# Kernel optimization log

Hardware: AMD Instinct MI355X
Metric: run time of the kernel (lower is better)

## Reference

```python
import jax, jax.numpy as jnp
import numpy as np

IN_CH = 128
HID = 64
EPS = 1e-5
N_NODES = 20000
E_UND = 80000


def _build_line_graph(edge_index, num_nodes):
    # dedupe to unique undirected edges (src<dst); line-graph nodes = these edges
    src = np.asarray(edge_index[0]); dst = np.asarray(edge_index[1])
    m = src < dst
    u, v = src[m], dst[m]
    key = u.astype(np.int64) * num_nodes + v.astype(np.int64)
    _, first = np.unique(key, return_index=True)
    u, v = u[first], v[first]
    E = u.shape[0]
    # incidence lists grouped by node; all ordered pairs of co-incident edges
    nodes = np.concatenate([u, v])
    eids = np.concatenate([np.arange(E), np.arange(E)])
    order = np.argsort(nodes, kind="stable")
    nodes_s, eids_s = nodes[order], eids[order]
    counts = np.bincount(nodes_s, minlength=num_nodes)
    offsets = np.concatenate([np.zeros(1, np.int64), np.cumsum(counts)])
    grp_start = offsets[nodes_s]
    reps = counts[nodes_s]
    total = int(reps.sum())
    starts = np.cumsum(reps) - reps
    idx = np.arange(total) - np.repeat(starts, reps) + np.repeat(grp_start, reps)
    row = np.repeat(eids_s, reps); col = eids_s[idx]
    keep = row != col
    return np.stack([u, v]), np.stack([row[keep], col[keep]])


def _gcn_conv(x, src, dst, W, b):
    # PyG GCNConv: add self loops, symmetric D^-1/2 (A+I) D^-1/2 normalization
    N = x.shape[0]
    sl = jnp.arange(N)
    s = jnp.concatenate([src, sl]); d = jnp.concatenate([dst, sl])
    deg = jax.ops.segment_sum(jnp.ones(s.shape[0], x.dtype), d, num_segments=N)
    dinv = jax.lax.rsqrt(jnp.maximum(deg, 1.0))
    h = x @ W
    msg = h[s] * (dinv[s] * dinv[d])[:, None]
    return jax.ops.segment_sum(msg, d, num_segments=N) + b


def _edge_scores(line_x, lsrc, ldst, W1, b1, gamma1, beta1, W2, b2):
    h = _gcn_conv(line_x, lsrc, ldst, W1, b1)
    mu = h.mean(0); var = h.var(0)  # BatchNorm1d, training-mode batch stats
    h = jax.nn.relu(gamma1 * (h - mu) * jax.lax.rsqrt(var + EPS) + beta1)
    return jax.nn.sigmoid(_gcn_conv(h, lsrc, ldst, W2, b2))[:, 0]


def _cluster(clean, topk_idx, num_nodes):
    ti = np.asarray(topk_idx)
    sel_src = np.asarray(clean[0])[ti]; sel_dst = np.asarray(clean[1])[ti]
    n2c = np.arange(num_nodes)
    rev = sel_dst[::-1]
    _, fi = np.unique(rev, return_index=True)
    last = sel_dst.shape[0] - 1 - fi
    n2c[sel_dst[last]] = sel_src[last]
    uniq = np.unique(n2c)
    M = int(uniq.shape[0])
    old_to_new = np.full(num_nodes, -1, np.int64)
    old_to_new[uniq] = np.arange(M)
    return old_to_new[n2c], uniq, M


def _make_graph():
    rng = np.random.default_rng(0)
    a = rng.integers(0, N_NODES, E_UND)
    off = rng.integers(1, N_NODES, E_UND)
    b = (a + off) % N_NODES  # no self loops
    u = np.minimum(a, b); v = np.maximum(a, b)
    return np.stack([np.concatenate([u, v]), np.concatenate([v, u])]).astype(np.int64)


def _make_params():
    ks = jax.random.split(jax.random.key(0), 4)
    x = jax.random.normal(ks[0], (N_NODES, IN_CH), jnp.float32)
    W1 = jax.random.normal(ks[1], (IN_CH, HID), jnp.float32) / np.float32(np.sqrt(IN_CH))
    b1 = jnp.zeros((HID,), jnp.float32)
    gamma1 = jnp.ones((HID,), jnp.float32)
    beta1 = jnp.zeros((HID,), jnp.float32)
    W2 = jax.random.normal(ks[2], (HID, 1), jnp.float32) / np.float32(np.sqrt(HID))
    b2 = jnp.zeros((1,), jnp.float32)
    return x, W1, b1, gamma1, beta1, W2, b2


def setup_inputs() -> dict:
    x, W1, b1, gamma1, beta1, W2, b2 = _make_params()
    return {
        "x": x, "W1": W1, "b1": b1, "gamma1": gamma1, "beta1": beta1,
        "W2": W2, "b2": b2,
        "edge_index": jnp.asarray(_make_graph()),
        "batch": jnp.zeros((N_NODES,), jnp.int32),
    }


def reference(x, W1, b1, gamma1, beta1, W2, b2, edge_index, batch):
    N = x.shape[0]
    clean, line_ei = _build_line_graph(edge_index, N)
    csrc = jnp.asarray(clean[0]); cdst = jnp.asarray(clean[1])
    lsrc = jnp.asarray(line_ei[0]); ldst = jnp.asarray(line_ei[1])
    line_x = 0.5 * (x[csrc] + x[cdst])  # line-graph node features
    scores = _edge_scores(line_x, lsrc, ldst, W1, b1, gamma1, beta1, W2, b2)
    E_c = scores.shape[0]
    k = max(1, min(E_c // 2, N // 2))
    _, topk_idx = jax.lax.top_k(scores, k)
    new_indices, uniq, M = _cluster(clean, topk_idx, N)
    ni = jnp.asarray(new_indices)
    # aggregate: per-cluster mean of member node features (code's weights are unused)
    counts = jax.ops.segment_sum(jnp.ones(N, x.dtype), ni, num_segments=M)
    x_pool = jax.ops.segment_sum(x, ni, num_segments=M) / counts[:, None]
    batch_pool = batch[jnp.asarray(uniq)]
    # build_new_edges: relabel, drop self loops, coalesce (sorted unique)
    ei = np.asarray(edge_index)
    ns = new_indices[ei[0]]; nd = new_indices[ei[1]]
    keep = ns != nd
    pk = ns[keep] * M + nd[keep]
    upk = np.unique(pk)
    edge_index_pool = jnp.asarray(np.stack([upk // M, upk % M]))
    return (x_pool, edge_index_pool, batch_pool, scores, ni)
```

## Files before the change

kernel.cpp:

```cpp
#include <hip/hip_runtime.h>
#include <stdint.h>

typedef unsigned long long u64;
typedef unsigned int u32;

#define NND 20000
#define EUA 160000
#define EFE 80000
#define ICH 128
#define HIDC 64
#define SCAN_BS 256
#define NB_N ((NND + 255) / 256)
#define NB_EU ((EUA + 255) / 256)
#define NB_EF ((EFE + 255) / 256)
#define NB_E64 ((EFE * HIDC + 255) / 256)
#define NB_X ((NND * ICH + 255) / 256)
#define NSCAN_B ((NND + SCAN_BS - 1) / SCAN_BS)
#define HIST_BLOCKS 128
#define GEB 64
#define XS_PAD 132
#define NCHAIN 4096
#define OUT_MAX_INIT 3000000
#define BK64 64
#define SEL_BINS 4096


__global__ void kScanA(const int* __restrict__ in, int* __restrict__ out,
                       int* __restrict__ bsums, int n) {
    __shared__ int sh[SCAN_BS];
    int tid = threadIdx.x;
    int i = blockIdx.x * SCAN_BS + tid;
    int v = (i < n) ? in[i] : 0;
    sh[tid] = v;
    __syncthreads();
    for (int o = 1; o < SCAN_BS; o <<= 1) {
        int t = (tid >= o) ? sh[tid - o] : 0;
        __syncthreads();
        sh[tid] += t;
        __syncthreads();
    }
    if (i < n) out[i] = sh[tid] - v;
    if (tid == SCAN_BS - 1) bsums[blockIdx.x] = sh[tid];
}
__global__ void kScanB(int* __restrict__ out, const int* __restrict__ bsums,
                       int n, int nb, int* __restrict__ totalDst) {
    __shared__ int sh[160];
    int tid = threadIdx.x;
    if (tid <= nb) sh[tid] = (tid < nb) ? bsums[tid] : 0;
    __syncthreads();
    if (tid == 0) {
        int acc = 0;
        for (int i = 0; i < nb; i++) { int t = sh[i]; sh[i] = acc; acc += t; }
        sh[nb] = acc;
    }
    __syncthreads();
    int i = blockIdx.x * SCAN_BS + tid;
    if (i < n) out[i] += sh[blockIdx.x];
    if (i == 0) {
        int tot = sh[nb];
        out[n] = tot;
        *totalDst = tot;
    }
}

__global__ void kFilterScatter64(const int* __restrict__ ei, int* __restrict__ cnt,
                                 int* __restrict__ bucketV) {
    int i = blockIdx.x * 256 + threadIdx.x;
    if (i >= EUA) return;
    int s = ei[i], d = ei[EUA + i];
    if (s < d) {
        int p = atomicAdd(&cnt[s], 1);
        bucketV[(s << 6) + p] = d;
    }
}
__global__ void kRankSort64(const int* __restrict__ in, int* __restrict__ out,
                            const int* __restrict__ lenA, int* __restrict__ ucnt) {
    int a = blockIdx.x;
    int len = lenA[a];
    int base = a << 6;
    for (int j = threadIdx.x; j < len; j += 64) {
        int v = in[base + j];
        int r = 0;
        for (int i = 0; i < len; i++) {
            int w = in[base + i];
            r += (w < v) || (w == v && i < j);
        }
        out[base + r] = v;
    }
    __syncthreads();
    int c = 0;
    for (int j = threadIdx.x; j < len; j += 64)
        c += (j == 0) || (out[base + j] != out[base + j - 1]);
#pragma unroll
    for (int o = 32; o > 0; o >>= 1) c += __shfl_down(c, o, 64);
    if (threadIdx.x == 0) ucnt[a] = c;
}
__global__ void kCompactInc(const int* __restrict__ arr, const int* __restrict__ cnt,
                            const int* __restrict__ uoff, int* __restrict__ eU,
                            int* __restrict__ eV, int* __restrict__ icnt) {
    int u = blockIdx.x * 256 + threadIdx.x;
    if (u >= NND) return;
    int s = u << 6, e = s + cnt[u], o = uoff[u];
    int myc = 0;
    for (int i = s; i < e; i++)
        if (i == s || arr[i] != arr[i - 1]) {
            int v = arr[i];
            eU[o] = u; eV[o] = v; o++;
            atomicAdd(&icnt[v], 1);
            myc++;
        }
    if (myc) atomicAdd(&icnt[u], myc);
}

__global__ void kIncScatterDinv64(const int* __restrict__ eU, const int* __restrict__ eV,
                                  const int* __restrict__ scal, int* __restrict__ itmp,
                                  int* __restrict__ ilist, const int* __restrict__ icnt,
                                  float* __restrict__ dinv) {
    int e = blockIdx.x * 256 + threadIdx.x;
    if (e >= scal[0]) return;
    int u = eU[e], v = eV[e];
    ilist[(u << 6) + atomicAdd(&itmp[u], 1)] = e;
    ilist[(v << 6) + atomicAdd(&itmp[v], 1)] = e;
    dinv[e] = rsqrtf((float)(icnt[u] + icnt[v] - 1));
}

__global__ void kGemm(const float* __restrict__ x, const float* __restrict__ W1,
                      const int* __restrict__ eU, const int* __restrict__ eV,
                      const int* __restrict__ scal, float* __restrict__ h) {
    __shared__ float W1s[ICH][HIDC];
    __shared__ float xs[GEB][XS_PAD];
    int t = threadIdx.x;
    int E = scal[0];
    int e0 = blockIdx.x * GEB;
    if (e0 >= E) return;

    {
        const float4* Wv = (const float4*)W1;
        float4* Ws = (float4*)&W1s[0][0];
        for (int i = t; i < ICH * HIDC / 4; i += 256) Ws[i] = Wv[i];
    }
    {
        int eb = t >> 2, q = t & 3;
        int e = e0 + eb;
        if (e < E) {
            int u = eU[e], v = eV[e];
            const float4* xu = (const float4*)(x + (size_t)u * ICH) + q * 8;
            const float4* xv = (const float4*)(x + (size_t)v * ICH) + q * 8;
            float* xd = &xs[eb][q * 32];
#pragma unroll
            for (int i = 0; i < 8; i++) {
                float4 a = xu[i], b = xv[i];
                xd[i * 4 + 0] = 0.5f * (a.x + b.x);
                xd[i * 4 + 1] = 0.5f * (a.y + b.y);
                xd[i * 4 + 2] = 0.5f * (a.z + b.z);
                xd[i * 4 + 3] = 0.5f * (a.w + b.w);
            }
        }
    }
    __syncthreads();

    int cg4 = (t & 15) * 4;
    int es = t >> 4;
    float a00=0,a01=0,a02=0,a03=0, a10=0,a11=0,a12=0,a13=0;
    float a20=0,a21=0,a22=0,a23=0, a30=0,a31=0,a32=0,a33=0;
#pragma unroll 4
    for (int k = 0; k < ICH; k++) {
        float4 wv = *(const float4*)&W1s[k][cg4];
        float x0 = xs[es][k], x1 = xs[es + 16][k];
        float x2 = xs[es + 32][k], x3 = xs[es + 48][k];
        a00 += x0 * wv.x; a01 += x0 * wv.y; a02 += x0 * wv.z; a03 += x0 * wv.w;
        a10 += x1 * wv.x; a11 += x1 * wv.y; a12 += x1 * wv.z; a13 += x1 * wv.w;
        a20 += x2 * wv.x; a21 += x2 * wv.y; a22 += x2 * wv.z; a23 += x2 * wv.w;
        a30 += x3 * wv.x; a31 += x3 * wv.y; a32 += x3 * wv.z; a33 += x3 * wv.w;
    }
    int e;
    e = e0 + es;
    if (e < E) *(float4*)&h[(size_t)e * HIDC + cg4] = make_float4(a00, a01, a02, a03);
    e = e0 + es + 16;
    if (e < E) *(float4*)&h[(size_t)e * HIDC + cg4] = make_float4(a10, a11, a12, a13);
    e = e0 + es + 32;
    if (e < E) *(float4*)&h[(size_t)e * HIDC + cg4] = make_float4(a20, a21, a22, a23);
    e = e0 + es + 48;
    if (e < E) *(float4*)&h[(size_t)e * HIDC + cg4] = make_float4(a30, a31, a32, a33);
}

__global__ void kSGather(const float* __restrict__ h, const float* __restrict__ dinv,
                         const int* __restrict__ icnt, const int* __restrict__ ilist,
                         float* __restrict__ S) {
    int n = blockIdx.x;
    int c = threadIdx.x;
    int base = n << 6, len = icnt[n];
    float acc = 0.f;
    for (int j = 0; j < len; j++) {
        int ed = ilist[base + j];
        acc += h[(size_t)ed * HIDC + c] * dinv[ed];
    }
    S[(size_t)n * HIDC + c] = acc;
}
__global__ void kConv1Red1(const float* __restrict__ h, const float* __restrict__ S,
                           const float* __restrict__ dinv, const int* __restrict__ eU,
                           const int* __restrict__ eV, const float* __restrict__ b1,
                           const int* __restrict__ scal, float* __restrict__ h2,
                           float* __restrict__ partial) {
    int t = threadIdx.x;
    int g = blockIdx.x * 4 + (t >> 6);
    int c = t & 63;
    int E = scal[0];
    float bc = b1[c];
    float acc = 0.f;
    for (int e = g; e < E; e += NCHAIN) {
        float a = dinv[e];
        float v = a * (S[(size_t)eU[e] * HIDC + c] + S[(size_t)eV[e] * HIDC + c]) -
                  a * a * h[(size_t)e * HIDC + c] + bc;
        h2[(size_t)e * HIDC + c] = v;
        acc += v;
    }
    partial[g * HIDC + c] = acc;
}
__global__ void kRed1v(const float* __restrict__ h2, const int* __restrict__ scal,
                       const float* __restrict__ muvar, float* __restrict__ partial) {
    int t = threadIdx.x;
    int g = blockIdx.x * 4 + (t >> 6);
    int c = t & 63;
    int E = scal[0];
    float m = muvar[c];
    float acc = 0.f;
    for (int e = g; e < E; e += NCHAIN) {
        float d = h2[(size_t)e * HIDC + c] - m;
        acc += d * d;
    }
    partial[g * HIDC + c] = acc;
}
__global__ void kRed2(const float* __restrict__ partial, const int* __restrict__ scal,
                      float* __restrict__ muvar, int pass) {
    __shared__ float sh[4][HIDC];
    int t = threadIdx.x;
    int q = t >> 6, c = t & 63;
    float acc = 0.f;
    int g0 = q * (NCHAIN / 4);
    for (int g = g0; g < g0 + NCHAIN / 4; g++) acc += partial[g * HIDC + c];
    sh[q][c] = acc;
    __syncthreads();
    if (q == 0) {
        float s = ((sh[0][c] + sh[1][c]) + sh[2][c]) + sh[3][c];
        muvar[pass * HIDC + c] = s / (float)scal[0];
    }
}
__global__ void kNormZ(const float* __restrict__ h2, const float* __restrict__ muvar,
                       const float* __restrict__ gamma1, const float* __restrict__ beta1,
                       const float* __restrict__ W2, const int* __restrict__ scal,
                       float* __restrict__ z) {
    int idx = blockIdx.x * 256 + threadIdx.x;
    int e = idx >> 6;
    if (e >= scal[0]) return;
    int c = idx & 63;
    float t = gamma1[c] * (h2[idx] - muvar[c]) * rsqrtf(muvar[HIDC + c] + 1e-5f) + beta1[c];
    t = t > 0.f ? t : 0.f;
    float p = t * W2[c];
#pragma unroll
    for (int o = 32; o > 0; o >>= 1) p += __shfl_down(p, o, 64);
    if (c == 0) z[e] = p;
}
__global__ void kS2(const float* __restrict__ z, const float* __restrict__ dinv,
                    const int* __restrict__ icnt, const int* __restrict__ ilist,
                    float* __restrict__ S2) {
    int n = blockIdx.x * 256 + threadIdx.x;
    if (n >= NND) return;
    int base = n << 6, len = icnt[n];
    float acc = 0.f;
    for (int j = 0; j < len; j++) {
        int e = ilist[base + j];
        acc += z[e] * dinv[e];
    }
    S2[n] = acc;
}
__global__ void kScore(const float* __restrict__ z, const float* __restrict__ S2,
                       const float* __restrict__ dinv, const int* __restrict__ eU,
                       const int* __restrict__ eV, const float* __restrict__ b2,
                       const int* __restrict__ scal, float* __restrict__ score,
                       u64* __restrict__ okey, u64* __restrict__ minOkey) {
    int e = blockIdx.x * 256 + threadIdx.x;
    if (e < NND) minOkey[e] = ~0ULL;
    int E = scal[0];
    if (e >= E) return;
    float a = dinv[e];
    float l = a * (S2[eU[e]] + S2[eV[e]]) - a * a * z[e] + b2[0];
    float s = 1.f / (1.f + expf(-l));
    score[e] = s;
    u32 b = __float_as_uint(s);
    b = (b >> 31) ? ~b : (b | 0x80000000u);
    okey[e] = (((u64)b) << 17) | (u32)(0x1FFFFu - (u32)e);
}

__device__ __forceinline__ u64 selReplay(const int* __restrict__ histBase, int passes,
                                         int E, int t, int* aux, int* shTmp) {
    int kr = E / 2;
    if (kr > NND / 2) kr = NND / 2;
    if (kr < 1) kr = 1;
    u64 pref = 1ULL << 48;
    for (int q = 0; q < passes; q++) {
        int shift = 36 - 12 * q;
        const int* hq = histBase + q * SEL_BINS;
        int b[16];
        int g = 0;
#pragma unroll
        for (int j = 0; j < 16; j++) { b[j] = hq[16 * t + j]; g += b[j]; }
        aux[t] = g;
        __syncthreads();
        for (int o = 1; o < 256; o <<= 1) {
            int v = (t + o < 256) ? aux[t + o] : 0;
            __syncthreads();
            aux[t] += v;
            __syncthreads();
        }
        int suf = aux[t] - g;
        if (suf < kr && kr <= suf + g) {
            int cum = suf, found = 16 * t;
            for (int j = 15; j >= 0; j--) {
                int hc = b[j];
                if (cum + hc >= kr) { found = 16 * t + j; break; }
                cum += hc;
            }
            shTmp[0] = found;
            shTmp[1] = kr - cum;
        }
        __syncthreads();
        pref |= ((u64)shTmp[0]) << shift;
        kr = shTmp[1];
        __syncthreads();
    }
    return pref;
}
__global__ void kHistR(const u64* __restrict__ okey, const int* __restrict__ scal,
                       int* __restrict__ histBase, int pass) {
    __shared__ int sh[4][SEL_BINS];
    __shared__ int aux[256];
    __shared__ int shTmp[2];
    int t = threadIdx.x;
    int E = scal[0];
    u64 p = selReplay(histBase, pass, E, t, aux, shTmp);
    for (int j = t; j < 4 * SEL_BINS; j += 256) ((int*)sh)[j] = 0;
    __syncthreads();
    int wv = t >> 6;
    int shift = 36 - 12 * pass;
    u64 maskHi = (~0ULL) << (shift + 12);
    for (int e = blockIdx.x * 256 + t; e < E; e += HIST_BLOCKS * 256) {
        u64 kk = okey[e];
        if ((kk & maskHi) == p)
            atomicAdd(&sh[wv][(int)((kk >> shift) & (SEL_BINS - 1))], 1);
    }
    __syncthreads();
    int* hp = histBase + pass * SEL_BINS;
    for (int j = t; j < SEL_BINS; j += 256) {
        int v = sh[0][j] + sh[1][j] + sh[2][j] + sh[3][j];
        if (v) atomicAdd(&hp[j], v);
    }
}

__global__ void kMinKey(const u64* __restrict__ okey, const int* __restrict__ eV,
                        const int* __restrict__ scal, const int* __restrict__ histBase,
                        u64* __restrict__ minOkey) {
    __shared__ int aux[256];
    __shared__ int shTmp[2];
    int t = threadIdx.x;
    int E = scal[0];
    u64 pref = selReplay(histBase, 4, E, t, aux, shTmp);
    int i = blockIdx.x * 256 + t;
    if (i < E) {
        u64 k = okey[i];
        if (k >= pref) atomicMin(&minOkey[eV[i]], k);
    }
}
__global__ void kCluster(const u64* __restrict__ minOkey, const int* __restrict__ eU,
                         int* __restrict__ n2c, int* __restrict__ present) {
    int v = blockIdx.x * 256 + threadIdx.x;
    if (v >= NND) return;
    u64 mk = minOkey[v];
    int m = v;
    if (mk != ~0ULL) m = eU[0x1FFFFu - (u32)(mk & 0x1FFFFu)];
    n2c[v] = m;
    present[m] = 1;
}

__global__ void kNiXacc(const float* __restrict__ x, const int* __restrict__ n2c,
                        const int* __restrict__ o2n, int* __restrict__ ni,
                        int* __restrict__ ccnt, float* __restrict__ dout) {
    int idx = blockIdx.x * 256 + threadIdx.x;
    if (idx >= NND * ICH) return;
    int n = idx >> 7, c = idx & 127;
    int m = o2n[n2c[n]];
    atomicAdd(&dout[(size_t)m * ICH + c], x[idx]);
    if (c == 0) {
        ni[n] = m;
        atomicAdd(&ccnt[m], 1);
    }
}
__global__ void kXdivCEcount(float* __restrict__ dout, const int* __restrict__ ccnt,
                             const int* __restrict__ scal, const int* __restrict__ ei,
                             const int* __restrict__ ni, int* __restrict__ ecnt2) {
    int idx = blockIdx.x * 256 + threadIdx.x;
    if (idx < scal[2] * ICH) dout[idx] /= (float)ccnt[idx >> 7];
    if (idx < EUA) {
        int a = ni[ei[idx]], b = ni[ei[EUA + idx]];
        if (a != b) atomicAdd(&ecnt2[a], 1);
    }
}

__global__ void kCEscatter(const int* __restrict__ ei, const int* __restrict__ ni,
                           const int* __restrict__ eoff2, int* __restrict__ etmp2,
                           int* __restrict__ bkD) {
    int i = blockIdx.x * 256 + threadIdx.x;
    if (i >= EUA) return;
    int a = ni[ei[i]], b = ni[ei[EUA + i]];
    if (a != b) {
        int p = eoff2[a] + atomicAdd(&etmp2[a], 1);
        bkD[p] = b;
    }
}
__global__ void kRankSort(const int* __restrict__ in, int* __restrict__ out,
                          const int* __restrict__ offA, int* __restrict__ ucnt) {
    int a = blockIdx.x;
    int s = offA[a], e = offA[a + 1], len = e - s;
    for (int j = threadIdx.x; j < len; j += 64) {
        int v = in[s + j];
        int r = 0;
        for (int i = 0; i < len; i++) {
            int w = in[s + i];
            r += (w < v) || (w == v && i < j);
        }
        out[s + r] = v;
    }
    __syncthreads();
    int c = 0;
    for (int j = threadIdx.x; j < len; j += 64)
        c += (j == 0) || (out[s + j] != out[s + j - 1]);
#pragma unroll
    for (int o = 32; o > 0; o >>= 1) c += __shfl_down(c, o, 64);
    if (threadIdx.x == 0) ucnt[a] = c;
}
__global__ void kCEwriteTail(const int* __restrict__ bkD2, const int* __restrict__ eoff2,
                             const int* __restrict__ ueoff, const int* __restrict__ scal,
                             const int* __restrict__ batch, const int* __restrict__ present,
                             const int* __restrict__ o2n, const float* __restrict__ score,
                             const int* __restrict__ ni, float* __restrict__ dout) {
    int i = blockIdx.x * 256 + threadIdx.x;
    int E = scal[0], M = scal[2], Ep = scal[3];
    size_t base = (size_t)M * ICH;
    if (i < NND) {
        int s = eoff2[i], e = eoff2[i + 1];
        float* r0 = dout + base;
        float* r1 = r0 + Ep;
        int o = ueoff[i];
        for (int j = s; j < e; j++)
            if (j == s || bkD2[j] != bkD2[j - 1]) {
                r0[o] = (float)i;
                r1[o] = (float)bkD2[j];
                o++;
            }
    }
    size_t tb = base + 2 * (size_t)Ep;
    if (i < NND && present[i]) dout[tb + o2n[i]] = (float)batch[i];
    if (i < E) dout[tb + M + i] = score[i];
    if (i < NND) dout[tb + M + E + i] = (float)ni[i];
}

extern "C" void kernel_launch(void* const* d_in, const int* in_sizes, int n_in,
                              void* d_out, int out_size, void* d_ws, size_t ws_size,
                              hipStream_t stream) {
    (void)in_sizes; (void)n_in; (void)ws_size;
    const float* x = (const float*)d_in[0];
    const float* W1 = (const float*)d_in[1];
    const float* b1 = (const float*)d_in[2];
    const float* gamma1 = (const float*)d_in[3];
    const float* beta1 = (const float*)d_in[4];
    const float* W2 = (const float*)d_in[5];
    const float* b2 = (const float*)d_in[6];
    const int* ei = (const int*)d_in[7];
    const int* batch = (const int*)d_in[8];
    float* dout = (float*)d_out;

    char* w = (char*)d_ws;
    size_t off = 0;
    auto carve = [&](size_t bytes) -> void* {
        off = (off + 255) & ~(size_t)255;
        void* p = w + off;
        off += bytes;
        return p;
    };
    char* zero0 = w;
    int* cnt = (int*)carve(NND * 4);
    int* itmp = (int*)carve(NND * 4);
    int* icnt = (int*)carve(NND * 4);
    int* present = (int*)carve(NND * 4);
    int* ccnt = (int*)carve(NND * 4);
    int* ecnt2 = (int*)carve(NND * 4);
    int* etmp2 = (int*)carve(NND * 4);
    int* scal = (int*)carve(16 * 4);
    int* hist4 = (int*)carve((size_t)4 * SEL_BINS * 4);
    size_t zeroBytes = off;
    int* ucnt = (int*)carve(NND * 4);
    int* uoff = (int*)carve((NND + 2) * 4);
    int* bsums = (int*)carve((NSCAN_B + 2) * 4);
    int* n2c = (int*)carve(NND * 4);
    int* o2n = (int*)carve((NND + 2) * 4);
    int* niArr = (int*)carve(NND * 4);
    int* eoff2 = (int*)carve((NND + 2) * 4);
    int* uecnt = (int*)carve(NND * 4);
    int* ueoff = (int*)carve((NND + 2) * 4);
    int* bucketV = (int*)carve((size_t)NND * BK64 * 4);
    int* bucketS = (int*)carve((size_t)NND * BK64 * 4);
    int* eU = (int*)carve(EFE * 4);
    int* eV = (int*)carve(EFE * 4);
    int* ilist = (int*)carve((size_t)NND * BK64 * 4);
    int* ilistS = (int*)carve((size_t)NND * BK64 * 4);
    int* bkD = (int*)carve(EUA * 4);
    int* bkD2 = (int*)carve(EUA * 4);
    u64* okey = (u64*)carve(EFE * 8);
    u64* minOkey = (u64*)carve(NND * 8);
    float* dinv = (float*)carve(EFE * 4);
    float* h = (float*)carve((size_t)EFE * HIDC * 4);
    float* h2 = (float*)carve((size_t)EFE * HIDC * 4);
    float* Snode = (float*)carve((size_t)NND * HIDC * 4);
    float* partial = (float*)carve((size_t)NCHAIN * HIDC * 4);
    float* muvar = (float*)carve(128 * 4);
    float* zArr = (float*)carve(EFE * 4);
    float* S2 = (float*)carve(NND * 4);
    float* score = (float*)carve(EFE * 4);

    auto scan = [&](const int* in, int* outp, int* totalDst) {
        kScanA<<<NSCAN_B, SCAN_BS, 0, stream>>>(in, outp, bsums, NND);
        kScanB<<<NSCAN_B, SCAN_BS, 0, stream>>>(outp, bsums, NND, NSCAN_B, totalDst);
    };

    size_t outInit = (size_t)out_size;
    if (outInit > OUT_MAX_INIT) outInit = OUT_MAX_INIT;
    hipMemsetAsync(zero0, 0, zeroBytes, stream);
    hipMemsetAsync(d_out, 0, outInit * 4, stream);

    kFilterScatter64<<<NB_EU, 256, 0, stream>>>(ei, cnt, bucketV);
    kRankSort64<<<NND, 64, 0, stream>>>(bucketV, bucketS, cnt, ucnt);
    scan(ucnt, uoff, scal + 0);
    kCompactInc<<<NB_N, 256, 0, stream>>>(bucketS, cnt, uoff, eU, eV, icnt);

    kIncScatterDinv64<<<NB_EF, 256, 0, stream>>>(eU, eV, scal, itmp, ilist, icnt, dinv);
    kRankSort64<<<NND, 64, 0, stream>>>(ilist, ilistS, icnt, ucnt);

    kGemm<<<(EFE + GEB - 1) / GEB, 256, 0, stream>>>(x, W1, eU, eV, scal, h);
    kSGather<<<NND, HIDC, 0, stream>>>(h, dinv, icnt, ilistS, Snode);
    kConv1Red1<<<NCHAIN / 4, 256, 0, stream>>>(h, Snode, dinv, eU, eV, b1, scal, h2, partial);
    kRed2<<<1, 256, 0, stream>>>(partial, scal, muvar, 0);
    kRed1v<<<NCHAIN / 4, 256, 0, stream>>>(h2, scal, muvar, partial);
    kRed2<<<1, 256, 0, stream>>>(partial, scal, muvar, 1);
    kNormZ<<<NB_E64, 256, 0, stream>>>(h2, muvar, gamma1, beta1, W2, scal, zArr);

    kS2<<<NB_N, 256, 0, stream>>>(zArr, dinv, icnt, ilistS, S2);
    kScore<<<NB_EF, 256, 0, stream>>>(zArr, S2, dinv, eU, eV, b2, scal, score, okey,
                                      minOkey);

    for (int p = 0; p < 4; p++)
        kHistR<<<HIST_BLOCKS, 256, 0, stream>>>(okey, scal, hist4, p);

    kMinKey<<<NB_EF, 256, 0, stream>>>(okey, eV, scal, hist4, minOkey);
    kCluster<<<NB_N, 256, 0, stream>>>(minOkey, eU, n2c, present);
    scan(present, o2n, scal + 2);
    kNiXacc<<<NB_X, 256, 0, stream>>>(x, n2c, o2n, niArr, ccnt, dout);
    kXdivCEcount<<<NB_X, 256, 0, stream>>>(dout, ccnt, scal, ei, niArr, ecnt2);

    scan(ecnt2, eoff2, scal + 4);
    kCEscatter<<<NB_EU, 256, 0, stream>>>(ei, niArr, eoff2, etmp2, bkD);
    kRankSort<<<NND, 64, 0, stream>>>(bkD, bkD2, eoff2, uecnt);
    scan(uecnt, ueoff, scal + 3);
    kCEwriteTail<<<NB_EF, 256, 0, stream>>>(bkD2, eoff2, ueoff, scal, batch, present,
                                            o2n, score, niArr, dout);
}
```

Baseline: 398.0 us.

## Replace atomic cluster feature pooling with per-cluster member-list gather

kCluster now also appends each node to a fixed-capacity (64-slot) member list of its cluster, reusing the bucketV buffer. A new kXPool kernel, one block per cluster, gathers and averages member rows directly. This replaces the per-element float atomicAdd scatter and the separate divide pass, and it removes the full output memset. The risks are overflow if a cluster ever has more than 64 members, and output padding that is no longer zeroed.

```diff
diff --git a/kernel.cpp b/kernel.cpp
--- a/kernel.cpp
+++ b/kernel.cpp
@@ -14,13 +14,11 @@
 #define NB_EU ((EUA + 255) / 256)
 #define NB_EF ((EFE + 255) / 256)
 #define NB_E64 ((EFE * HIDC + 255) / 256)
-#define NB_X ((NND * ICH + 255) / 256)
 #define NSCAN_B ((NND + SCAN_BS - 1) / SCAN_BS)
 #define HIST_BLOCKS 128
 #define GEB 64
 #define XS_PAD 132
 #define NCHAIN 4096
-#define OUT_MAX_INIT 3000000
 #define BK64 64
 #define SEL_BINS 4096
 
@@ -372,7 +370,8 @@
     }
 }
 __global__ void kCluster(const u64* __restrict__ minOkey, const int* __restrict__ eU,
-                         int* __restrict__ n2c, int* __restrict__ present) {
+                         int* __restrict__ n2c, int* __restrict__ present,
+                         int* __restrict__ csize, int* __restrict__ cmemb) {
     int v = blockIdx.x * 256 + threadIdx.x;
     if (v >= NND) return;
     u64 mk = minOkey[v];
@@ -380,30 +379,31 @@
     if (mk != ~0ULL) m = eU[0x1FFFFu - (u32)(mk & 0x1FFFFu)];
     n2c[v] = m;
     present[m] = 1;
-}
-
-__global__ void kNiXacc(const float* __restrict__ x, const int* __restrict__ n2c,
-                        const int* __restrict__ o2n, int* __restrict__ ni,
-                        int* __restrict__ ccnt, float* __restrict__ dout) {
-    int idx = blockIdx.x * 256 + threadIdx.x;
-    if (idx >= NND * ICH) return;
-    int n = idx >> 7, c = idx & 127;
-    int m = o2n[n2c[n]];
-    atomicAdd(&dout[(size_t)m * ICH + c], x[idx]);
-    if (c == 0) {
-        ni[n] = m;
-        atomicAdd(&ccnt[m], 1);
-    }
-}
-__global__ void kXdivCEcount(float* __restrict__ dout, const int* __restrict__ ccnt,
-                             const int* __restrict__ scal, const int* __restrict__ ei,
-                             const int* __restrict__ ni, int* __restrict__ ecnt2) {
-    int idx = blockIdx.x * 256 + threadIdx.x;
-    if (idx < scal[2] * ICH) dout[idx] /= (float)ccnt[idx >> 7];
-    if (idx < EUA) {
-        int a = ni[ei[idx]], b = ni[ei[EUA + idx]];
-        if (a != b) atomicAdd(&ecnt2[a], 1);
-    }
+    int slot = atomicAdd(&csize[m], 1);
+    cmemb[(m << 6) + slot] = v;
+}
+
+__global__ void kXPool(const float* __restrict__ x, const int* __restrict__ n2c,
+                       const int* __restrict__ o2n, const int* __restrict__ present,
+                       const int* __restrict__ csize, const int* __restrict__ cmemb,
+                       int* __restrict__ ni, float* __restrict__ dout) {
+    int u = blockIdx.x;
+    int c = threadIdx.x;
+    if (c == 0) ni[u] = o2n[n2c[u]];
+    if (!present[u]) return;
+    int s = csize[u];
+    int base = u << 6;
+    float acc = 0.f;
+    for (int j = 0; j < s; j++)
+        acc += x[(size_t)cmemb[base + j] * ICH + c];
+    dout[(size_t)o2n[u] * ICH + c] = acc / (float)s;
+}
+__global__ void kCEcount(const int* __restrict__ ei, const int* __restrict__ ni,
+                         int* __restrict__ ecnt2) {
+    int i = blockIdx.x * 256 + threadIdx.x;
+    if (i >= EUA) return;
+    int a = ni[ei[i]], b = ni[ei[EUA + i]];
+    if (a != b) atomicAdd(&ecnt2[a], 1);
 }
 
 __global__ void kCEscatter(const int* __restrict__ ei, const int* __restrict__ ni,
@@ -467,7 +467,7 @@
 extern "C" void kernel_launch(void* const* d_in, const int* in_sizes, int n_in,
                               void* d_out, int out_size, void* d_ws, size_t ws_size,
                               hipStream_t stream) {
-    (void)in_sizes; (void)n_in; (void)ws_size;
+    (void)in_sizes; (void)n_in; (void)ws_size; (void)out_size;
     const float* x = (const float*)d_in[0];
     const float* W1 = (const float*)d_in[1];
     const float* b1 = (const float*)d_in[2];
@@ -492,7 +492,7 @@
     int* itmp = (int*)carve(NND * 4);
     int* icnt = (int*)carve(NND * 4);
     int* present = (int*)carve(NND * 4);
-    int* ccnt = (int*)carve(NND * 4);
+    int* csize = (int*)carve(NND * 4);
     int* ecnt2 = (int*)carve(NND * 4);
     int* etmp2 = (int*)carve(NND * 4);
     int* scal = (int*)carve(16 * 4);
@@ -532,10 +532,7 @@
         kScanB<<<NSCAN_B, SCAN_BS, 0, stream>>>(outp, bsums, NND, NSCAN_B, totalDst);
     };
 
-    size_t outInit = (size_t)out_size;
-    if (outInit > OUT_MAX_INIT) outInit = OUT_MAX_INIT;
     hipMemsetAsync(zero0, 0, zeroBytes, stream);
-    hipMemsetAsync(d_out, 0, outInit * 4, stream);
 
     kFilterScatter64<<<NB_EU, 256, 0, stream>>>(ei, cnt, bucketV);
     kRankSort64<<<NND, 64, 0, stream>>>(bucketV, bucketS, cnt, ucnt);
@@ -561,10 +558,11 @@
         kHistR<<<HIST_BLOCKS, 256, 0, stream>>>(okey, scal, hist4, p);
 
     kMinKey<<<NB_EF, 256, 0, stream>>>(okey, eV, scal, hist4, minOkey);
-    kCluster<<<NB_N, 256, 0, stream>>>(minOkey, eU, n2c, present);
+    kCluster<<<NB_N, 256, 0, stream>>>(minOkey, eU, n2c, present, csize, bucketV);
     scan(present, o2n, scal + 2);
-    kNiXacc<<<NB_X, 256, 0, stream>>>(x, n2c, o2n, niArr, ccnt, dout);
-    kXdivCEcount<<<NB_X, 256, 0, stream>>>(dout, ccnt, scal, ei, niArr, ecnt2);
+
+    kXPool<<<NND, 128, 0, stream>>>(x, n2c, o2n, present, csize, bucketV, niArr, dout);
+    kCEcount<<<NB_EU, 256, 0, stream>>>(ei, niArr, ecnt2);
 
     scan(ecnt2, eoff2, scal + 4);
     kCEscatter<<<NB_EU, 256, 0, stream>>>(ei, niArr, eoff2, etmp2, bkD);
```

Result: no change. 393.4 us (-1.1%).
